# Optimization experiments

Hardware: AMD Instinct MI355X
Metric: run time of the kernel (lower is better)

## Reference

```python
import jax, jax.numpy as jnp
import numpy as np

N_LOC = 100000
N_EVT = 100000
N_EDGE = 1600000
F_LOC = 128
F_EVT = 128
QID_DIM = 16
QID_BUCKETS = 4096
HID = 64


def setup_inputs() -> dict:
    key = jax.random.key(0)
    ks = jax.random.split(key, 16)
    s = 0.05
    emb = jax.random.normal(ks[4], (QID_BUCKETS + 1, QID_DIM), jnp.float32) * s
    emb = emb.at[0].set(0.0)  # padding_idx=0
    return {
        "loc_feat": jax.random.normal(ks[0], (N_LOC, F_LOC), jnp.float32),
        "evt_feat": jax.random.normal(ks[1], (N_EVT, F_EVT), jnp.float32),
        "qid_bucket": jax.random.randint(ks[2], (N_LOC,), 0, QID_BUCKETS + 1),
        "edge_index": jax.random.randint(ks[3], (2, N_EDGE), 0, N_LOC),
        "emb": emb,
        "W_loc": jax.random.normal(ks[5], (F_LOC + QID_DIM, HID), jnp.float32) * s,
        "b_loc": jnp.zeros((HID,), jnp.float32),
        "W_evt": jax.random.normal(ks[6], (F_EVT, HID), jnp.float32) * s,
        "b_evt": jnp.zeros((HID,), jnp.float32),
        "W_l": jax.random.normal(ks[7], (HID, HID), jnp.float32) * s,
        "b_l": jnp.zeros((HID,), jnp.float32),
        "W_r": jax.random.normal(ks[8], (HID, HID), jnp.float32) * s,
        "W_h1": jax.random.normal(ks[9], (HID, HID // 2), jnp.float32) * s,
        "b_h1": jnp.zeros((HID // 2,), jnp.float32),
        "W_h2": jax.random.normal(ks[10], (HID // 2, 1), jnp.float32) * s,
        "b_h2": jnp.zeros((1,), jnp.float32),
    }


def reference(loc_feat, evt_feat, qid_bucket, edge_index, emb,
              W_loc, b_loc, W_evt, b_evt, W_l, b_l, W_r,
              W_h1, b_h1, W_h2, b_h2):
    # location input = [x || qid_embedding]
    loc_in = jnp.concatenate([loc_feat, emb[qid_bucket]], axis=1)
    loc_x = jax.nn.relu(loc_in @ W_loc + b_loc)          # [N_loc, H]
    evt_x = jax.nn.relu(evt_feat @ W_evt + b_evt)        # [N_evt, H]

    src, dst = edge_index[0], edge_index[1]
    msg = evt_x[src]                                     # [E, H] gather
    summed = jax.ops.segment_sum(msg, dst, num_segments=N_LOC)
    cnt = jax.ops.segment_sum(jnp.ones((msg.shape[0],), msg.dtype), dst,
                              num_segments=N_LOC)
    mean = summed / jnp.maximum(cnt, 1.0)[:, None]       # scatter-mean aggr

    # SAGEConv: lin_l(mean of neighbors) + lin_r(self)
    loc_x = jax.nn.relu(mean @ W_l + b_l + loc_x @ W_r)

    h = jax.nn.relu(loc_x @ W_h1 + b_h1)
    logits = (h @ W_h2 + b_h2)[:, 0]
    return logits
```

## Files before the change

### kernel.cpp

```cpp
#include <hip/hip_runtime.h>

#define N_LOC 100000
#define N_EVT 100000
#define N_EDGE 1600000
#define NB 391
#define NBIN 391
#define BCAPP 9216
#define TILE 4096
#define RBLK 64
#define DGRID 1563

typedef short bf16x8 __attribute__((ext_vector_type(8)));
typedef float f32x4  __attribute__((ext_vector_type(4)));

__device__ __forceinline__ unsigned bf16_rne(float x) {
    unsigned u = __float_as_uint(x);
    return (u + 0x7fffu + ((u >> 16) & 1u)) >> 16;
}
__device__ __forceinline__ float bf_lo(unsigned u) { return __uint_as_float(u << 16); }
__device__ __forceinline__ float bf_hi(unsigned u) { return __uint_as_float(u & 0xffff0000u); }

__global__ __launch_bounds__(256) void k_prep(
    const float* __restrict__ W_evt, const float* __restrict__ W_loc,
    const float* __restrict__ W_l, const float* __restrict__ W_r,
    const float* __restrict__ W_h1,
    unsigned short* __restrict__ Wt_evt,
    unsigned short* __restrict__ Wt_loc,
    unsigned short* __restrict__ Wt_c,
    unsigned short* __restrict__ Wt_h1,
    unsigned* __restrict__ dummy_row)
{
    const int t = threadIdx.x;
    for (int idx = t; idx < 64 * 64; idx += 256) {
        int kp = idx >> 6, c = idx & 63;
        *(unsigned*)&Wt_evt[c * 128 + 2 * kp] =
            bf16_rne(W_evt[(2 * kp + 0) * 64 + c]) |
            (bf16_rne(W_evt[(2 * kp + 1) * 64 + c]) << 16);
    }
    for (int idx = t; idx < 80 * 64; idx += 256) {
        int kp = idx >> 6, c = idx & 63;
        unsigned v = 0;
        if (kp < 72)
            v = bf16_rne(W_loc[(2 * kp + 0) * 64 + c]) |
                (bf16_rne(W_loc[(2 * kp + 1) * 64 + c]) << 16);
        *(unsigned*)&Wt_loc[c * 160 + 2 * kp] = v;
    }
    for (int idx = t; idx < 64 * 64; idx += 256) {
        int kp = idx >> 6, c = idx & 63;
        float w0, w1;
        if (kp < 32) { w0 = W_l[(2 * kp + 0) * 64 + c]; w1 = W_l[(2 * kp + 1) * 64 + c]; }
        else { w0 = W_r[(2 * kp - 64 + 0) * 64 + c]; w1 = W_r[(2 * kp - 64 + 1) * 64 + c]; }
        *(unsigned*)&Wt_c[c * 128 + 2 * kp] = bf16_rne(w0) | (bf16_rne(w1) << 16);
    }
    for (int idx = t; idx < 32 * 32; idx += 256) {
        int kp = idx >> 5, c = idx & 31;
        *(unsigned*)&Wt_h1[c * 64 + 2 * kp] =
            bf16_rne(W_h1[(2 * kp + 0) * 32 + c]) |
            (bf16_rne(W_h1[(2 * kp + 1) * 32 + c]) << 16);
    }
    if (t < 32) dummy_row[t] = 0u;
}

__global__ __launch_bounds__(256) void k_front(
    const float* __restrict__ evt_feat, const unsigned short* __restrict__ Wt_evt,
    const float* __restrict__ b_evt, unsigned short* __restrict__ evtb,
    const float* __restrict__ loc_feat, const int* __restrict__ qid,
    const float* __restrict__ emb, const unsigned short* __restrict__ Wt_loc,
    const float* __restrict__ b_loc, unsigned short* __restrict__ locxb,
    const int* __restrict__ ei, int* __restrict__ cntm, int* __restrict__ offm,
    unsigned* __restrict__ binned)
{
    __shared__ __align__(16) unsigned char smem[21504];
    const int bid = blockIdx.x;
    const int t = threadIdx.x;

    if (bid < NBIN) {
        int* h  = (int*)smem;
        int* sh = (int*)(smem + 1600);
        for (int i = t; i < NB; i += 256) h[i] = 0;
        __syncthreads();
        const int e0 = bid * TILE;
        int srcv[16], dstv[16], rnk[16];
#pragma unroll
        for (int j = 0; j < 16; ++j) {
            int e = e0 + j * 256 + t;
            if (e < N_EDGE) {
                srcv[j] = ei[e];
                dstv[j] = ei[N_EDGE + e];
                rnk[j] = atomicAdd(&h[dstv[j] >> 8], 1);
            }
        }
        __syncthreads();
        sh[t] = (t < NB) ? h[t] : 0;
        sh[t + 256] = (t + 256 < NB) ? h[t + 256] : 0;
        __syncthreads();
        for (int off = 1; off < 512; off <<= 1) {
            int v0 = (t >= off) ? sh[t - off] : 0;
            int v1 = (t + 256 >= off) ? sh[t + 256 - off] : 0;
            __syncthreads();
            sh[t] += v0;
            sh[t + 256] += v1;
            __syncthreads();
        }
        for (int i = t; i < NB; i += 256) {
            cntm[(size_t)bid * NB + i] = h[i];
            offm[(size_t)bid * NB + i] = sh[i] - h[i];
        }
#pragma unroll
        for (int j = 0; j < 16; ++j) {
            int e = e0 + j * 256 + t;
            if (e < N_EDGE) {
                int bk = dstv[j] >> 8;
                binned[(size_t)bid * TILE + (sh[bk] - h[bk]) + rnk[j]] =
                    (unsigned)srcv[j] | ((unsigned)(dstv[j] & 255) << 24);
            }
        }
        return;
    }

    const int lane = t & 63;
    const int w = t >> 6;
    const int colL = lane & 15;
    const int kq = lane >> 4;

    int db = bid - NBIN;
    if (db < DGRID) {
        unsigned short* sA = (unsigned short*)smem;
        const int gbase = db * RBLK;
        for (int idx = t; idx < RBLK * 32; idx += 256) {
            int row = idx >> 5, c4 = idx & 31;
            int grow = gbase + row;
            float4 v = (grow < N_EVT) ? ((const float4*)evt_feat)[(size_t)grow * 32 + c4]
                                      : make_float4(0.f, 0.f, 0.f, 0.f);
            uint2 p = make_uint2(bf16_rne(v.x) | (bf16_rne(v.y) << 16),
                                 bf16_rne(v.z) | (bf16_rne(v.w) << 16));
            *(uint2*)&sA[row * 136 + c4 * 4] = p;
        }
        __syncthreads();
        f32x4 acc0 = {0.f, 0.f, 0.f, 0.f}, acc1 = acc0, acc2 = acc0, acc3 = acc0;
#pragma unroll
        for (int s = 0; s < 4; ++s) {
            const int kb = s * 32 + kq * 8;
            bf16x8 a  = *(const bf16x8*)&sA[(16 * w + colL) * 136 + kb];
            bf16x8 b0 = *(const bf16x8*)&Wt_evt[(colL +  0) * 128 + kb];
            bf16x8 b1 = *(const bf16x8*)&Wt_evt[(colL + 16) * 128 + kb];
            bf16x8 b2 = *(const bf16x8*)&Wt_evt[(colL + 32) * 128 + kb];
            bf16x8 b3 = *(const bf16x8*)&Wt_evt[(colL + 48) * 128 + kb];
            acc0 = __builtin_amdgcn_mfma_f32_16x16x32_bf16(a, b0, acc0, 0, 0, 0);
            acc1 = __builtin_amdgcn_mfma_f32_16x16x32_bf16(a, b1, acc1, 0, 0, 0);
            acc2 = __builtin_amdgcn_mfma_f32_16x16x32_bf16(a, b2, acc2, 0, 0, 0);
            acc3 = __builtin_amdgcn_mfma_f32_16x16x32_bf16(a, b3, acc3, 0, 0, 0);
        }
        const float bias0 = b_evt[colL +  0];
        const float bias1 = b_evt[colL + 16];
        const float bias2 = b_evt[colL + 32];
        const float bias3 = b_evt[colL + 48];
        const int rbase = gbase + 16 * w + kq * 4;
#pragma unroll
        for (int j = 0; j < 4; ++j) {
            int grow = rbase + j;
            if (grow < N_EVT) {
                size_t o = (size_t)grow * 64;
                evtb[o + colL +  0] = (unsigned short)bf16_rne(fmaxf(acc0[j] + bias0, 0.f));
                evtb[o + colL + 16] = (unsigned short)bf16_rne(fmaxf(acc1[j] + bias1, 0.f));
                evtb[o + colL + 32] = (unsigned short)bf16_rne(fmaxf(acc2[j] + bias2, 0.f));
                evtb[o + colL + 48] = (unsigned short)bf16_rne(fmaxf(acc3[j] + bias3, 0.f));
            }
        }
        return;
    }

    {
        db -= DGRID;
        unsigned short* sA = (unsigned short*)smem;
        const int gbase = db * RBLK;
        for (int idx = t; idx < RBLK * 32; idx += 256) {
            int row = idx >> 5, c4 = idx & 31;
            int grow = gbase + row;
            float4 v = (grow < N_LOC) ? ((const float4*)loc_feat)[(size_t)grow * 32 + c4]
                                      : make_float4(0.f, 0.f, 0.f, 0.f);
            uint2 p = make_uint2(bf16_rne(v.x) | (bf16_rne(v.y) << 16),
                                 bf16_rne(v.z) | (bf16_rne(v.w) << 16));
            *(uint2*)&sA[row * 168 + c4 * 4] = p;
        }
        for (int idx = t; idx < RBLK * 4; idx += 256) {
            int row = idx >> 2, e4 = idx & 3;
            int grow = gbase + row;
            int q = (grow < N_LOC) ? qid[grow] : 0;
            float4 v = ((const float4*)emb)[(size_t)q * 4 + e4];
            uint2 p = make_uint2(bf16_rne(v.x) | (bf16_rne(v.y) << 16),
                                 bf16_rne(v.z) | (bf16_rne(v.w) << 16));
            *(uint2*)&sA[row * 168 + 128 + e4 * 4] = p;
        }
        for (int idx = t; idx < RBLK * 2; idx += 256) {
            int row = idx >> 1, h2 = idx & 1;
            *(uint4*)&sA[row * 168 + 144 + h2 * 8] = make_uint4(0, 0, 0, 0);
        }
        __syncthreads();
        f32x4 acc0 = {0.f, 0.f, 0.f, 0.f}, acc1 = acc0, acc2 = acc0, acc3 = acc0;
#pragma unroll
        for (int s = 0; s < 5; ++s) {
            const int kb = s * 32 + kq * 8;
            bf16x8 a  = *(const bf16x8*)&sA[(16 * w + colL) * 168 + kb];
            bf16x8 b0 = *(const bf16x8*)&Wt_loc[(colL +  0) * 160 + kb];
            bf16x8 b1 = *(const bf16x8*)&Wt_loc[(colL + 16) * 160 + kb];
            bf16x8 b2 = *(const bf16x8*)&Wt_loc[(colL + 32) * 160 + kb];
            bf16x8 b3 = *(const bf16x8*)&Wt_loc[(colL + 48) * 160 + kb];
            acc0 = __builtin_amdgcn_mfma_f32_16x16x32_bf16(a, b0, acc0, 0, 0, 0);
            acc1 = __builtin_amdgcn_mfma_f32_16x16x32_bf16(a, b1, acc1, 0, 0, 0);
            acc2 = __builtin_amdgcn_mfma_f32_16x16x32_bf16(a, b2, acc2, 0, 0, 0);
            acc3 = __builtin_amdgcn_mfma_f32_16x16x32_bf16(a, b3, acc3, 0, 0, 0);
        }
        const float bias0 = b_loc[colL +  0];
        const float bias1 = b_loc[colL + 16];
        const float bias2 = b_loc[colL + 32];
        const float bias3 = b_loc[colL + 48];
        const int rbase = gbase + 16 * w + kq * 4;
#pragma unroll
        for (int j = 0; j < 4; ++j) {
            int grow = rbase + j;
            if (grow < N_LOC) {
                size_t o = (size_t)grow * 64;
                locxb[o + colL +  0] = (unsigned short)bf16_rne(fmaxf(acc0[j] + bias0, 0.f));
                locxb[o + colL + 16] = (unsigned short)bf16_rne(fmaxf(acc1[j] + bias1, 0.f));
                locxb[o + colL + 32] = (unsigned short)bf16_rne(fmaxf(acc2[j] + bias2, 0.f));
                locxb[o + colL + 48] = (unsigned short)bf16_rne(fmaxf(acc3[j] + bias3, 0.f));
            }
        }
    }
}

__global__ __launch_bounds__(256) void k_bfill(const int* __restrict__ cntm,
                                               const int* __restrict__ offm,
                                               const unsigned* __restrict__ binned,
                                               int* __restrict__ deg,
                                               int* __restrict__ row_ex,
                                               int* __restrict__ csr) {
    __shared__ int cnt0[NBIN];
    __shared__ int off0[NBIN];
    __shared__ int degl[256];
    __shared__ int sc[256];
    __shared__ int cur[256];
    const int b = blockIdx.x;
    const int t = threadIdx.x;
    for (int i = t; i < NBIN; i += 256) {
        cnt0[i] = cntm[(size_t)i * NB + b];
        off0[i] = offm[(size_t)i * NB + b];
    }
    degl[t] = 0;
    __syncthreads();
    for (int blk = t; blk < NBIN; blk += 256) {
        const int c = cnt0[blk];
        const unsigned* s = binned + (size_t)blk * TILE + off0[blk];
        for (int j = 0; j < c; ++j) atomicAdd(&degl[s[j] >> 24], 1);
    }
    __syncthreads();
    const int v = degl[t];
    const int vpad = (v + 15) & ~15;
    sc[t] = vpad;
    __syncthreads();
    for (int off = 1; off < 256; off <<= 1) {
        int x = (t >= off) ? sc[t - off] : 0;
        __syncthreads();
        sc[t] += x;
        __syncthreads();
    }
    const int ex = b * BCAPP + sc[t] - vpad;
    const int loc = b * 256 + t;
    if (loc < N_LOC) { deg[loc] = v; row_ex[loc] = ex; }
    cur[t] = ex;
    __syncthreads();
    for (int blk = t; blk < NBIN; blk += 256) {
        const int c = cnt0[blk];
        const unsigned* s = binned + (size_t)blk * TILE + off0[blk];
        for (int j = 0; j < c; ++j) {
            unsigned u = s[j];
            int pos = atomicAdd(&cur[u >> 24], 1);
            csr[pos] = (int)(u & 0x00FFFFFFu);
        }
    }
    for (int j = v; j < vpad; ++j) csr[ex + j] = N_EVT;
}

__global__ __launch_bounds__(256, 8) void k_aggr(const unsigned* __restrict__ evtb,
                                                 const int* __restrict__ row_ex,
                                                 const int* __restrict__ deg,
                                                 const int* __restrict__ csr,
                                                 unsigned* __restrict__ meanb, int n) {
    const int lane = threadIdx.x & 63;
    int wid = (blockIdx.x * 256 + threadIdx.x) >> 6;
    wid = __builtin_amdgcn_readfirstlane(wid);
    if (wid >= n) return;
    const int beg = row_ex[wid];
    const int cnt = deg[wid];
    const int cntp = (cnt + 15) & ~15;
    const int half = lane >> 5;
    const int c = lane & 31;
    float a0 = 0.0f, a1 = 0.0f;
    for (int i = 0; i < cntp; i += 16) {
        const int bb = beg + i + half;
        int s0 = csr[bb +  0];
        int s1 = csr[bb +  2];
        int s2 = csr[bb +  4];
        int s3 = csr[bb +  6];
        int s4 = csr[bb +  8];
        int s5 = csr[bb + 10];
        int s6 = csr[bb + 12];
        int s7 = csr[bb + 14];
        unsigned u0 = evtb[(size_t)s0 * 32 + c];
        unsigned u1 = evtb[(size_t)s1 * 32 + c];
        unsigned u2 = evtb[(size_t)s2 * 32 + c];
        unsigned u3 = evtb[(size_t)s3 * 32 + c];
        unsigned u4 = evtb[(size_t)s4 * 32 + c];
        unsigned u5 = evtb[(size_t)s5 * 32 + c];
        unsigned u6 = evtb[(size_t)s6 * 32 + c];
        unsigned u7 = evtb[(size_t)s7 * 32 + c];
        a0 += ((bf_lo(u0) + bf_lo(u1)) + (bf_lo(u2) + bf_lo(u3))) +
              ((bf_lo(u4) + bf_lo(u5)) + (bf_lo(u6) + bf_lo(u7)));
        a1 += ((bf_hi(u0) + bf_hi(u1)) + (bf_hi(u2) + bf_hi(u3))) +
              ((bf_hi(u4) + bf_hi(u5)) + (bf_hi(u6) + bf_hi(u7)));
    }
    a0 += __shfl_xor(a0, 32);
    a1 += __shfl_xor(a1, 32);
    const float inv = 1.0f / (float)max(cnt, 1);
    if (lane < 32)
        meanb[(size_t)wid * 32 + c] = bf16_rne(a0 * inv) | (bf16_rne(a1 * inv) << 16);
}

__global__ __launch_bounds__(256) void k_comb(
    const unsigned* __restrict__ meanb, const unsigned* __restrict__ locxb,
    const unsigned short* __restrict__ Wt_c, const float* __restrict__ b_l,
    const unsigned short* __restrict__ Wt_h1, const float* __restrict__ b_h1,
    const float* __restrict__ W_h2, const float* __restrict__ b_h2,
    float* __restrict__ out, int n)
{
    __shared__ unsigned short sA[64 * 136];
    __shared__ unsigned short sX[64 * 72];
    const int t = threadIdx.x;
    const int gbase = blockIdx.x * RBLK;
    for (int idx = t; idx < RBLK * 32; idx += 256) {
        int row = idx >> 5, q = idx & 31;
        int grow = gbase + row;
        uint2 p = make_uint2(0, 0);
        if (grow < n) {
            p = (q < 16) ? ((const uint2*)meanb)[(size_t)grow * 16 + q]
                         : ((const uint2*)locxb)[(size_t)grow * 16 + (q - 16)];
        }
        *(uint2*)&sA[row * 136 + q * 4] = p;
    }
    __syncthreads();
    const int lane = t & 63;
    const int w = t >> 6;
    const int colL = lane & 15;
    const int kq = lane >> 4;
    f32x4 acc0 = {0.f, 0.f, 0.f, 0.f}, acc1 = acc0, acc2 = acc0, acc3 = acc0;
#pragma unroll
    for (int s = 0; s < 4; ++s) {
        const int kb = s * 32 + kq * 8;
        bf16x8 a  = *(const bf16x8*)&sA[(16 * w + colL) * 136 + kb];
        bf16x8 b0 = *(const bf16x8*)&Wt_c[(colL +  0) * 128 + kb];
        bf16x8 b1 = *(const bf16x8*)&Wt_c[(colL + 16) * 128 + kb];
        bf16x8 b2 = *(const bf16x8*)&Wt_c[(colL + 32) * 128 + kb];
        bf16x8 b3 = *(const bf16x8*)&Wt_c[(colL + 48) * 128 + kb];
        acc0 = __builtin_amdgcn_mfma_f32_16x16x32_bf16(a, b0, acc0, 0, 0, 0);
        acc1 = __builtin_amdgcn_mfma_f32_16x16x32_bf16(a, b1, acc1, 0, 0, 0);
        acc2 = __builtin_amdgcn_mfma_f32_16x16x32_bf16(a, b2, acc2, 0, 0, 0);
        acc3 = __builtin_amdgcn_mfma_f32_16x16x32_bf16(a, b3, acc3, 0, 0, 0);
    }
    {
        const float bias0 = b_l[colL +  0];
        const float bias1 = b_l[colL + 16];
        const float bias2 = b_l[colL + 32];
        const float bias3 = b_l[colL + 48];
#pragma unroll
        for (int j = 0; j < 4; ++j) {
            int row = 16 * w + kq * 4 + j;
            sX[row * 72 + colL +  0] = (unsigned short)bf16_rne(fmaxf(acc0[j] + bias0, 0.f));
            sX[row * 72 + colL + 16] = (unsigned short)bf16_rne(fmaxf(acc1[j] + bias1, 0.f));
            sX[row * 72 + colL + 32] = (unsigned short)bf16_rne(fmaxf(acc2[j] + bias2, 0.f));
            sX[row * 72 + colL + 48] = (unsigned short)bf16_rne(fmaxf(acc3[j] + bias3, 0.f));
        }
    }
    f32x4 h0 = {0.f, 0.f, 0.f, 0.f}, h1 = h0;
#pragma unroll
    for (int s = 0; s < 2; ++s) {
        const int kb = s * 32 + kq * 8;
        bf16x8 a  = *(const bf16x8*)&sX[(16 * w + colL) * 72 + kb];
        bf16x8 b0 = *(const bf16x8*)&Wt_h1[(colL +  0) * 64 + kb];
        bf16x8 b1 = *(const bf16x8*)&Wt_h1[(colL + 16) * 64 + kb];
        h0 = __builtin_amdgcn_mfma_f32_16x16x32_bf16(a, b0, h0, 0, 0, 0);
        h1 = __builtin_amdgcn_mfma_f32_16x16x32_bf16(a, b1, h1, 0, 0, 0);
    }
    {
        const float bh1c0 = b_h1[colL];
        const float bh1c1 = b_h1[colL + 16];
        const float wh2c0 = W_h2[colL];
        const float wh2c1 = W_h2[colL + 16];
        const float bh2 = b_h2[0];
#pragma unroll
        for (int j = 0; j < 4; ++j) {
            float p = fmaxf(h0[j] + bh1c0, 0.f) * wh2c0 +
                      fmaxf(h1[j] + bh1c1, 0.f) * wh2c1;
            p += __shfl_xor(p, 1);
            p += __shfl_xor(p, 2);
            p += __shfl_xor(p, 4);
            p += __shfl_xor(p, 8);
            int grow = gbase + 16 * w + kq * 4 + j;
            if (colL == 0 && grow < n) out[grow] = p + bh2;
        }
    }
}

extern "C" void kernel_launch(void* const* d_in, const int* in_sizes, int n_in,
                              void* d_out, int out_size, void* d_ws, size_t ws_size,
                              hipStream_t stream) {
    const float* loc_feat = (const float*)d_in[0];
    const float* evt_feat = (const float*)d_in[1];
    const int*   qid      = (const int*)d_in[2];
    const int*   ei       = (const int*)d_in[3];
    const float* emb      = (const float*)d_in[4];
    const float* W_loc    = (const float*)d_in[5];
    const float* b_loc    = (const float*)d_in[6];
    const float* W_evt    = (const float*)d_in[7];
    const float* b_evt    = (const float*)d_in[8];
    const float* W_l      = (const float*)d_in[9];
    const float* b_l      = (const float*)d_in[10];
    const float* W_r      = (const float*)d_in[11];
    const float* W_h1     = (const float*)d_in[12];
    const float* b_h1     = (const float*)d_in[13];
    const float* W_h2     = (const float*)d_in[14];
    const float* b_h2     = (const float*)d_in[15];
    float* out = (float*)d_out;

    char* ws = (char*)d_ws;
    size_t off = 0;
    auto alloc = [&](size_t bytes) -> void* {
        void* p = ws + off;
        off += (bytes + 255) & ~(size_t)255;
        return p;
    };
    unsigned* evtb  = (unsigned*)alloc((size_t)(N_EVT + 1) * 32 * 4);
    unsigned* locxb = (unsigned*)alloc((size_t)N_LOC * 32 * 4);
    unsigned* meanb = (unsigned*)alloc((size_t)N_LOC * 32 * 4);
    unsigned* binned= (unsigned*)alloc((size_t)NBIN * TILE * 4);
    int*   cntm     = (int*)alloc((size_t)NBIN * NB * 4);
    int*   offm     = (int*)alloc((size_t)NBIN * NB * 4);
    int*   deg      = (int*)alloc((size_t)N_LOC * 4);
    int*   row_ex   = (int*)alloc((size_t)(N_LOC + 1) * 4);
    int*   csr      = (int*)alloc((size_t)NB * BCAPP * 4);
    unsigned short* Wt_evt = (unsigned short*)alloc(64 * 128 * 2);
    unsigned short* Wt_loc = (unsigned short*)alloc(64 * 160 * 2);
    unsigned short* Wt_c   = (unsigned short*)alloc(64 * 128 * 2);
    unsigned short* Wt_h1  = (unsigned short*)alloc(32 * 64 * 2);
    (void)ws_size; (void)in_sizes; (void)n_in; (void)out_size;

    k_prep<<<1, 256, 0, stream>>>(W_evt, W_loc, W_l, W_r, W_h1,
                                  Wt_evt, Wt_loc, Wt_c, Wt_h1,
                                  evtb + (size_t)N_EVT * 32);
    k_front<<<NBIN + 2 * DGRID, 256, 0, stream>>>(
        evt_feat, Wt_evt, b_evt, (unsigned short*)evtb,
        loc_feat, qid, emb, Wt_loc, b_loc, (unsigned short*)locxb,
        ei, cntm, offm, binned);
    k_bfill<<<NB, 256, 0, stream>>>(cntm, offm, binned, deg, row_ex, csr);
    k_aggr<<<N_LOC / 4, 256, 0, stream>>>(evtb, row_ex, deg, csr, meanb, N_LOC);
    k_comb<<<DGRID, 256, 0, stream>>>(meanb, locxb, Wt_c, b_l, Wt_h1, b_h1,
                                      W_h2, b_h2, out, N_LOC);
}
```

Baseline: 148.8 us.

## Load MFMA A-fragments directly from global memory, bypassing LDS staging

The dense front and combine GEMMs now build their A operand fragments by reading fp32 (or bf16) rows straight from global memory into registers and converting them there, instead of staging tiles through shared memory behind a barrier. This shrinks k_front's LDS footprint to the histogram arrays only, which can raise occupancy, and the embedding part of the location GEMM is handled as a separate fifth K-step. The weight-prep kernel is also spread over 24 blocks instead of one. The trade-off is that global loads are less coalesced: each lane reads 32-byte pieces of a different row, and neighbouring lanes repeat reads of the same rows across K-steps.

```diff
diff --git a/kernel.cpp b/kernel.cpp
--- a/kernel.cpp
+++ b/kernel.cpp
@@ -19,6 +19,16 @@
 }
 __device__ __forceinline__ float bf_lo(unsigned u) { return __uint_as_float(u << 16); }
 __device__ __forceinline__ float bf_hi(unsigned u) { return __uint_as_float(u & 0xffff0000u); }
+
+__device__ __forceinline__ bf16x8 frag_from_f32(const float* p) {
+    float4 v0 = *(const float4*)p;
+    float4 v1 = *(const float4*)(p + 4);
+    uint4 pk = make_uint4(bf16_rne(v0.x) | (bf16_rne(v0.y) << 16),
+                          bf16_rne(v0.z) | (bf16_rne(v0.w) << 16),
+                          bf16_rne(v1.x) | (bf16_rne(v1.y) << 16),
+                          bf16_rne(v1.z) | (bf16_rne(v1.w) << 16));
+    return *(bf16x8*)&pk;
+}
 
 __global__ __launch_bounds__(256) void k_prep(
     const float* __restrict__ W_evt, const float* __restrict__ W_loc,
@@ -30,14 +40,15 @@
     unsigned short* __restrict__ Wt_h1,
     unsigned* __restrict__ dummy_row)
 {
-    const int t = threadIdx.x;
-    for (int idx = t; idx < 64 * 64; idx += 256) {
+    const int g0 = blockIdx.x * 256 + threadIdx.x;
+    const int gs = gridDim.x * 256;
+    for (int idx = g0; idx < 64 * 64; idx += gs) {
         int kp = idx >> 6, c = idx & 63;
         *(unsigned*)&Wt_evt[c * 128 + 2 * kp] =
             bf16_rne(W_evt[(2 * kp + 0) * 64 + c]) |
             (bf16_rne(W_evt[(2 * kp + 1) * 64 + c]) << 16);
     }
-    for (int idx = t; idx < 80 * 64; idx += 256) {
+    for (int idx = g0; idx < 80 * 64; idx += gs) {
         int kp = idx >> 6, c = idx & 63;
         unsigned v = 0;
         if (kp < 72)
@@ -45,20 +56,20 @@
                 (bf16_rne(W_loc[(2 * kp + 1) * 64 + c]) << 16);
         *(unsigned*)&Wt_loc[c * 160 + 2 * kp] = v;
     }
-    for (int idx = t; idx < 64 * 64; idx += 256) {
+    for (int idx = g0; idx < 64 * 64; idx += gs) {
         int kp = idx >> 6, c = idx & 63;
         float w0, w1;
         if (kp < 32) { w0 = W_l[(2 * kp + 0) * 64 + c]; w1 = W_l[(2 * kp + 1) * 64 + c]; }
         else { w0 = W_r[(2 * kp - 64 + 0) * 64 + c]; w1 = W_r[(2 * kp - 64 + 1) * 64 + c]; }
         *(unsigned*)&Wt_c[c * 128 + 2 * kp] = bf16_rne(w0) | (bf16_rne(w1) << 16);
     }
-    for (int idx = t; idx < 32 * 32; idx += 256) {
+    for (int idx = g0; idx < 32 * 32; idx += gs) {
         int kp = idx >> 5, c = idx & 31;
         *(unsigned*)&Wt_h1[c * 64 + 2 * kp] =
             bf16_rne(W_h1[(2 * kp + 0) * 32 + c]) |
             (bf16_rne(W_h1[(2 * kp + 1) * 32 + c]) << 16);
     }
-    if (t < 32) dummy_row[t] = 0u;
+    if (blockIdx.x == 0 && threadIdx.x < 32) dummy_row[threadIdx.x] = 0u;
 }
 
 __global__ __launch_bounds__(256) void k_front(
@@ -70,13 +81,12 @@
     const int* __restrict__ ei, int* __restrict__ cntm, int* __restrict__ offm,
     unsigned* __restrict__ binned)
 {
-    __shared__ __align__(16) unsigned char smem[21504];
+    __shared__ int h[NB];
+    __shared__ int sh[512];
     const int bid = blockIdx.x;
     const int t = threadIdx.x;
 
     if (bid < NBIN) {
-        int* h  = (int*)smem;
-        int* sh = (int*)(smem + 1600);
         for (int i = t; i < NB; i += 256) h[i] = 0;
         __syncthreads();
         const int e0 = bid * TILE;
@@ -125,23 +135,14 @@
 
     int db = bid - NBIN;
     if (db < DGRID) {
-        unsigned short* sA = (unsigned short*)smem;
         const int gbase = db * RBLK;
-        for (int idx = t; idx < RBLK * 32; idx += 256) {
-            int row = idx >> 5, c4 = idx & 31;
-            int grow = gbase + row;
-            float4 v = (grow < N_EVT) ? ((const float4*)evt_feat)[(size_t)grow * 32 + c4]
-                                      : make_float4(0.f, 0.f, 0.f, 0.f);
-            uint2 p = make_uint2(bf16_rne(v.x) | (bf16_rne(v.y) << 16),
-                                 bf16_rne(v.z) | (bf16_rne(v.w) << 16));
-            *(uint2*)&sA[row * 136 + c4 * 4] = p;
-        }
-        __syncthreads();
+        const int arow = min(gbase + 16 * w + colL, N_EVT - 1);
+        const float* frow = evt_feat + (size_t)arow * 128;
         f32x4 acc0 = {0.f, 0.f, 0.f, 0.f}, acc1 = acc0, acc2 = acc0, acc3 = acc0;
 #pragma unroll
         for (int s = 0; s < 4; ++s) {
             const int kb = s * 32 + kq * 8;
-            bf16x8 a  = *(const bf16x8*)&sA[(16 * w + colL) * 136 + kb];
+            bf16x8 a  = frag_from_f32(frow + kb);
             bf16x8 b0 = *(const bf16x8*)&Wt_evt[(colL +  0) * 128 + kb];
             bf16x8 b1 = *(const bf16x8*)&Wt_evt[(colL + 16) * 128 + kb];
             bf16x8 b2 = *(const bf16x8*)&Wt_evt[(colL + 32) * 128 + kb];
@@ -172,36 +173,33 @@
 
     {
         db -= DGRID;
-        unsigned short* sA = (unsigned short*)smem;
         const int gbase = db * RBLK;
-        for (int idx = t; idx < RBLK * 32; idx += 256) {
-            int row = idx >> 5, c4 = idx & 31;
-            int grow = gbase + row;
-            float4 v = (grow < N_LOC) ? ((const float4*)loc_feat)[(size_t)grow * 32 + c4]
-                                      : make_float4(0.f, 0.f, 0.f, 0.f);
-            uint2 p = make_uint2(bf16_rne(v.x) | (bf16_rne(v.y) << 16),
-                                 bf16_rne(v.z) | (bf16_rne(v.w) << 16));
-            *(uint2*)&sA[row * 168 + c4 * 4] = p;
-        }
-        for (int idx = t; idx < RBLK * 4; idx += 256) {
-            int row = idx >> 2, e4 = idx & 3;
-            int grow = gbase + row;
-            int q = (grow < N_LOC) ? qid[grow] : 0;
-            float4 v = ((const float4*)emb)[(size_t)q * 4 + e4];
-            uint2 p = make_uint2(bf16_rne(v.x) | (bf16_rne(v.y) << 16),
-                                 bf16_rne(v.z) | (bf16_rne(v.w) << 16));
-            *(uint2*)&sA[row * 168 + 128 + e4 * 4] = p;
-        }
-        for (int idx = t; idx < RBLK * 2; idx += 256) {
-            int row = idx >> 1, h2 = idx & 1;
-            *(uint4*)&sA[row * 168 + 144 + h2 * 8] = make_uint4(0, 0, 0, 0);
-        }
-        __syncthreads();
+        const int arow = min(gbase + 16 * w + colL, N_LOC - 1);
+        const float* frow = loc_feat + (size_t)arow * 128;
         f32x4 acc0 = {0.f, 0.f, 0.f, 0.f}, acc1 = acc0, acc2 = acc0, acc3 = acc0;
 #pragma unroll
-        for (int s = 0; s < 5; ++s) {
+        for (int s = 0; s < 4; ++s) {
             const int kb = s * 32 + kq * 8;
-            bf16x8 a  = *(const bf16x8*)&sA[(16 * w + colL) * 168 + kb];
+            bf16x8 a  = frag_from_f32(frow + kb);
+            bf16x8 b0 = *(const bf16x8*)&Wt_loc[(colL +  0) * 160 + kb];
+            bf16x8 b1 = *(const bf16x8*)&Wt_loc[(colL + 16) * 160 + kb];
+            bf16x8 b2 = *(const bf16x8*)&Wt_loc[(colL + 32) * 160 + kb];
+            bf16x8 b3 = *(const bf16x8*)&Wt_loc[(colL + 48) * 160 + kb];
+            acc0 = __builtin_amdgcn_mfma_f32_16x16x32_bf16(a, b0, acc0, 0, 0, 0);
+            acc1 = __builtin_amdgcn_mfma_f32_16x16x32_bf16(a, b1, acc1, 0, 0, 0);
+            acc2 = __builtin_amdgcn_mfma_f32_16x16x32_bf16(a, b2, acc2, 0, 0, 0);
+            acc3 = __builtin_amdgcn_mfma_f32_16x16x32_bf16(a, b3, acc3, 0, 0, 0);
+        }
+        {
+            const int kb = 128 + kq * 8;
+            bf16x8 a;
+            if (kq < 2) {
+                int q = qid[arow];
+                a = frag_from_f32(emb + (size_t)q * 16 + kq * 8);
+            } else {
+                uint4 z = make_uint4(0, 0, 0, 0);
+                a = *(bf16x8*)&z;
+            }
             bf16x8 b0 = *(const bf16x8*)&Wt_loc[(colL +  0) * 160 + kb];
             bf16x8 b1 = *(const bf16x8*)&Wt_loc[(colL + 16) * 160 + kb];
             bf16x8 b2 = *(const bf16x8*)&Wt_loc[(colL + 32) * 160 + kb];
@@ -334,30 +332,22 @@
     const float* __restrict__ W_h2, const float* __restrict__ b_h2,
     float* __restrict__ out, int n)
 {
-    __shared__ unsigned short sA[64 * 136];
     __shared__ unsigned short sX[64 * 72];
     const int t = threadIdx.x;
     const int gbase = blockIdx.x * RBLK;
-    for (int idx = t; idx < RBLK * 32; idx += 256) {
-        int row = idx >> 5, q = idx & 31;
-        int grow = gbase + row;
-        uint2 p = make_uint2(0, 0);
-        if (grow < n) {
-            p = (q < 16) ? ((const uint2*)meanb)[(size_t)grow * 16 + q]
-                         : ((const uint2*)locxb)[(size_t)grow * 16 + (q - 16)];
-        }
-        *(uint2*)&sA[row * 136 + q * 4] = p;
-    }
-    __syncthreads();
     const int lane = t & 63;
     const int w = t >> 6;
     const int colL = lane & 15;
     const int kq = lane >> 4;
+    const int arow = min(gbase + 16 * w + colL, n - 1);
+    const unsigned short* mrow = (const unsigned short*)meanb + (size_t)arow * 64;
+    const unsigned short* xrow = (const unsigned short*)locxb + (size_t)arow * 64;
     f32x4 acc0 = {0.f, 0.f, 0.f, 0.f}, acc1 = acc0, acc2 = acc0, acc3 = acc0;
 #pragma unroll
     for (int s = 0; s < 4; ++s) {
         const int kb = s * 32 + kq * 8;
-        bf16x8 a  = *(const bf16x8*)&sA[(16 * w + colL) * 136 + kb];
+        bf16x8 a = (s < 2) ? *(const bf16x8*)(mrow + kb)
+                           : *(const bf16x8*)(xrow + (kb - 64));
         bf16x8 b0 = *(const bf16x8*)&Wt_c[(colL +  0) * 128 + kb];
         bf16x8 b1 = *(const bf16x8*)&Wt_c[(colL + 16) * 128 + kb];
         bf16x8 b2 = *(const bf16x8*)&Wt_c[(colL + 32) * 128 + kb];
@@ -454,9 +444,9 @@
     unsigned short* Wt_h1  = (unsigned short*)alloc(32 * 64 * 2);
     (void)ws_size; (void)in_sizes; (void)n_in; (void)out_size;
 
-    k_prep<<<1, 256, 0, stream>>>(W_evt, W_loc, W_l, W_r, W_h1,
-                                  Wt_evt, Wt_loc, Wt_c, Wt_h1,
-                                  evtb + (size_t)N_EVT * 32);
+    k_prep<<<24, 256, 0, stream>>>(W_evt, W_loc, W_l, W_r, W_h1,
+                                   Wt_evt, Wt_loc, Wt_c, Wt_h1,
+                                   evtb + (size_t)N_EVT * 32);
     k_front<<<NBIN + 2 * DGRID, 256, 0, stream>>>(
         evt_feat, Wt_evt, b_evt, (unsigned short*)evtb,
         loc_feat, qid, emb, Wt_loc, b_loc, (unsigned short*)locxb,
```

Result: faster. 133.5 us (-10.2%).
